# Optimization experiments

Measured on AMD Instinct MI355X. Metric: run time of the kernel, lower is better.

Reference implementation:

```python
import jax, jax.numpy as jnp
import numpy as np

N_ENT = 15000  # entity id range; also used for relation ids in this synthetic setup

def _triple_key(h, r, t):
    # Unique int64 key per (h, r, t) triple; max ~15000^3 < 2^63.
    return (h * N_ENT + r) * N_ENT + t

def setup_inputs() -> dict:
    key = jax.random.key(0)
    k1, k2, k3, k4 = jax.random.split(key, 4)
    Q, N = 100000, 10000000
    heads = jax.random.randint(k1, (Q,), 0, N_ENT, dtype=jnp.int64)
    rels = jax.random.randint(k2, (Q,), 0, N_ENT, dtype=jnp.int64)
    tails = jax.random.randint(k3, (Q,), 0, N_ENT, dtype=jnp.int64)
    data = jax.random.randint(k4, (3, N), 0, N_ENT, dtype=jnp.int64)
    return {"heads": heads, "rels": rels, "tails": tails, "data": data}

def reference(heads, rels, tails, data) -> jnp.ndarray:
    # Faithful to PerfeCT.forward: response[i] = 1 iff (heads[i], rels[i], tails[i])
    # appears as a row of data.T; output = 10 * (response - 0.5).
    data_keys = jnp.sort(_triple_key(data[0], data[1], data[2]))  # [N]
    q_keys = _triple_key(heads, rels, tails)                       # [Q]
    idx = jnp.searchsorted(data_keys, q_keys)
    idx = jnp.clip(idx, 0, data_keys.shape[0] - 1)
    member = (data_keys[idx] == q_keys).astype(jnp.float32)        # [Q]
    return 10.0 * (member - 0.5)
```

## Files before the change

kernel.cpp:

```cpp
#include <hip/hip_runtime.h>
#include <stdint.h>


typedef int iv4 __attribute__((ext_vector_type(4)));

#define EMPTY  0xFFFFFFFFu
#define BWORDS 32768
#define QSLOTS 6
#define TPB    1024

static __device__ __forceinline__ uint32_t mix32(uint32_t x) {
    x ^= x >> 16; x *= 0x85ebca6bu;
    x ^= x >> 13; x *= 0xc2b2ae35u;
    x ^= x >> 16;
    return x;
}
static __device__ __forceinline__ uint32_t hash2(uint32_t x) {
    return mix32(x ^ 0x9E3779B9u);
}
static __device__ __forceinline__ uint32_t key32(int h, int r, int t) {
    return ((uint32_t)h * 15000u + (uint32_t)r) * 15000u + (uint32_t)t;
}
static __device__ __forceinline__ void bloom_wm(uint32_t key, uint32_t* w, uint32_t* m) {
    uint32_t z = mix32(key);
    *w = z & (BWORDS - 1u);
    *m = (1u << ((z >> 15) & 31u)) | (1u << ((z >> 20) & 31u));
}

__global__ void k_zero(uint32_t* __restrict__ p, int zeroWords, int totalWords) {
    int stride = gridDim.x * blockDim.x;
    for (int i = blockIdx.x * blockDim.x + threadIdx.x; i < totalWords; i += stride)
        p[i] = (i < zeroWords) ? 0u : EMPTY;
}

__global__ void k_insert(const int* __restrict__ qh, const int* __restrict__ qr,
                         const int* __restrict__ qt,
                         uint32_t* __restrict__ bloom, uint32_t* __restrict__ keys,
                         uint32_t tmask, int Q) {
    int i = blockIdx.x * blockDim.x + threadIdx.x;
    if (i >= Q) return;
    uint32_t key = key32(qh[i], qr[i], qt[i]);
    if (key == EMPTY) return;
    uint32_t w, m; bloom_wm(key, &w, &m);
    atomicOr(&bloom[w], m);
    uint32_t slot = hash2(key) & tmask;
    while (true) {
        uint32_t prev = atomicCAS(&keys[slot], EMPTY, key);
        if (prev == EMPTY || prev == key) return;
        slot = (slot + 1) & tmask;
    }
}

static __device__ __forceinline__ void probe_mark(uint32_t key,
                                                  const uint32_t* __restrict__ keys,
                                                  uint32_t* __restrict__ flagbits,
                                                  uint32_t tmask) {
    uint32_t slot = hash2(key) & tmask;
    while (true) {
        uint32_t v = keys[slot];
        if (v == key) { atomicOr(&flagbits[slot >> 5], 1u << (slot & 31)); return; }
        if (v == EMPTY) return;
        slot = (slot + 1) & tmask;
    }
}

__global__ __launch_bounds__(TPB) void k_scan(
        const int* __restrict__ dh, const int* __restrict__ dr,
        const int* __restrict__ dt,
        const uint32_t* __restrict__ bloom,
        const uint32_t* __restrict__ keys,
        uint32_t* __restrict__ flagbits, uint32_t* __restrict__ sent,
        uint32_t tmask, int nhex, int N) {
    __shared__ uint32_t lb[BWORDS];
    __shared__ uint32_t qb[TPB * QSLOTS];
    {
        const iv4* gb = (const iv4*)bloom;
        iv4* lb4 = (iv4*)lb;
        for (int i = threadIdx.x; i < BWORDS / 4; i += TPB) lb4[i] = gb[i];
    }
    __syncthreads();

    const iv4* H = (const iv4*)dh;
    const iv4* R = (const iv4*)dr;
    const iv4* T = (const iv4*)dt;
    int cnt = 0;
    int stride = gridDim.x * blockDim.x;

#define TESTQ(kk, vv, mm)                                                          \
    if ((kk) == EMPTY) *sent = 1u;                                                 \
    else if (((vv) & (mm)) == (mm)) {                                              \
        if (cnt < QSLOTS) { qb[cnt * TPB + threadIdx.x] = (kk); cnt++; }           \
        else probe_mark((kk), keys, flagbits, tmask);                              \
    }
#define GRP4(h4, r4, t4)                                                           \
    {                                                                              \
        uint32_t k0 = key32((h4).x, (r4).x, (t4).x), k1 = key32((h4).y, (r4).y, (t4).y); \
        uint32_t k2 = key32((h4).z, (r4).z, (t4).z), k3 = key32((h4).w, (r4).w, (t4).w); \
        uint32_t w0,m0,w1,m1,w2,m2,w3,m3;                                          \
        bloom_wm(k0,&w0,&m0); bloom_wm(k1,&w1,&m1);                                \
        bloom_wm(k2,&w2,&m2); bloom_wm(k3,&w3,&m3);                                \
        uint32_t v0 = lb[w0], v1 = lb[w1], v2 = lb[w2], v3 = lb[w3];               \
        TESTQ(k0, v0, m0) TESTQ(k1, v1, m1) TESTQ(k2, v2, m2) TESTQ(k3, v3, m3)    \
    }

    for (int j = blockIdx.x * blockDim.x + threadIdx.x; j < nhex; j += stride) {
        iv4 hA = H[j], hB = H[j + nhex], hC = H[j + 2 * nhex], hD = H[j + 3 * nhex];
        iv4 rA = R[j], rB = R[j + nhex], rC = R[j + 2 * nhex], rD = R[j + 3 * nhex];
        iv4 tA = T[j], tB = T[j + nhex], tC = T[j + 2 * nhex], tD = T[j + 3 * nhex];
        GRP4(hA, rA, tA) GRP4(hB, rB, tB) GRP4(hC, rC, tC) GRP4(hD, rD, tD)
    }
#undef GRP4
#undef TESTQ

    int rem = N - 16 * nhex;
    if (blockIdx.x == 0 && (int)threadIdx.x < rem) {
        int j = 16 * nhex + threadIdx.x;
        uint32_t k = key32(dh[j], dr[j], dt[j]);
        if (k == EMPTY) *sent = 1u;
        else probe_mark(k, keys, flagbits, tmask);
    }

    int m = cnt < QSLOTS ? cnt : QSLOTS;
    for (int c = 0; c < m; ++c)
        probe_mark(qb[c * TPB + threadIdx.x], keys, flagbits, tmask);
}

__global__ void k_out(const int* __restrict__ qh, const int* __restrict__ qr,
                      const int* __restrict__ qt,
                      const uint32_t* __restrict__ keys,
                      const uint32_t* __restrict__ flagbits,
                      const uint32_t* __restrict__ sent,
                      float* __restrict__ out, uint32_t tmask, int Q) {
    int i = blockIdx.x * blockDim.x + threadIdx.x;
    if (i >= Q) return;
    uint32_t key = key32(qh[i], qr[i], qt[i]);
    float v = -5.0f;
    if (key == EMPTY) {
        v = (*sent) ? 5.0f : -5.0f;
    } else {
        uint32_t slot = hash2(key) & tmask;
        while (true) {
            uint32_t kv = keys[slot];
            if (kv == key) { v = ((flagbits[slot >> 5] >> (slot & 31)) & 1u) ? 5.0f : -5.0f; break; }
            if (kv == EMPTY) break;
            slot = (slot + 1) & tmask;
        }
    }
    out[i] = v;
}

extern "C" void kernel_launch(void* const* d_in, const int* in_sizes, int n_in,
                              void* d_out, int out_size, void* d_ws, size_t ws_size,
                              hipStream_t stream) {
    const int* qh = (const int*)d_in[0];
    const int* qr = (const int*)d_in[1];
    const int* qt = (const int*)d_in[2];
    const int* data = (const int*)d_in[3];
    int Q = in_sizes[0];
    int N = in_sizes[3] / 3;
    const int* dh = data;
    const int* dr = data + (size_t)N;
    const int* dt = data + 2 * (size_t)N;
    float* out = (float*)d_out;

    int tb = 18;
    size_t bloomB = (size_t)BWORDS * 4;
    size_t need = bloomB + ((size_t)1 << (tb - 3)) + 256 + ((size_t)4 << tb);
    if (need > ws_size) tb = 17;
    size_t flagB = (size_t)1 << (tb - 3);
    uint32_t tmask = ((uint32_t)1 << tb) - 1u;

    uint32_t* bloom    = (uint32_t*)d_ws;
    uint32_t* flagbits = (uint32_t*)((char*)d_ws + bloomB);
    uint32_t* hdr      = (uint32_t*)((char*)d_ws + bloomB + flagB);
    uint32_t* keys     = (uint32_t*)((char*)d_ws + bloomB + flagB + 256);

    int zeroWords  = (int)((bloomB + flagB + 256) / 4);
    int totalWords = zeroWords + (1 << tb);
    k_zero<<<1024, 256, 0, stream>>>((uint32_t*)d_ws, zeroWords, totalWords);

    int qblocks = (Q + 255) / 256;
    k_insert<<<qblocks, 256, 0, stream>>>(qh, qr, qt, bloom, keys, tmask, Q);

    int nhex = N / 16;
    k_scan<<<256, TPB, 0, stream>>>(dh, dr, dt, bloom, keys, flagbits,
                                    hdr, tmask, nhex, N);

    k_out<<<qblocks, 256, 0, stream>>>(qh, qr, qt, keys, flagbits, hdr, out, tmask, Q);
}
```

Before: 222.0 us.

## Shrink bloom filter, keep probe queue in registers, raise scan occupancy

Halves the shared-memory bloom filter and replaces the shared-memory deferred-probe queue with six registers, so more scan blocks can reside per CU. The per-thread unroll drops from 16 to 8 elements, the grid doubles, and streaming loads use nontemporal hints. The goal is better latency hiding in the scan. The smaller bloom raises the false-positive rate, so more rows fall through to global hash-table probes.

```diff
diff --git a/kernel.cpp b/kernel.cpp
--- a/kernel.cpp
+++ b/kernel.cpp
@@ -5,8 +5,7 @@
 typedef int iv4 __attribute__((ext_vector_type(4)));
 
 #define EMPTY  0xFFFFFFFFu
-#define BWORDS 32768
-#define QSLOTS 6
+#define BWORDS 16384
 #define TPB    1024
 
 static __device__ __forceinline__ uint32_t mix32(uint32_t x) {
@@ -24,7 +23,7 @@
 static __device__ __forceinline__ void bloom_wm(uint32_t key, uint32_t* w, uint32_t* m) {
     uint32_t z = mix32(key);
     *w = z & (BWORDS - 1u);
-    *m = (1u << ((z >> 15) & 31u)) | (1u << ((z >> 20) & 31u));
+    *m = (1u << ((z >> 14) & 31u)) | (1u << ((z >> 19) & 31u));
 }
 
 __global__ void k_zero(uint32_t* __restrict__ p, int zeroWords, int totalWords) {
@@ -64,15 +63,14 @@
     }
 }
 
-__global__ __launch_bounds__(TPB) void k_scan(
+__global__ __launch_bounds__(TPB, 8) void k_scan(
         const int* __restrict__ dh, const int* __restrict__ dr,
         const int* __restrict__ dt,
         const uint32_t* __restrict__ bloom,
         const uint32_t* __restrict__ keys,
         uint32_t* __restrict__ flagbits, uint32_t* __restrict__ sent,
-        uint32_t tmask, int nhex, int N) {
+        uint32_t tmask, int n8, int N) {
     __shared__ uint32_t lb[BWORDS];
-    __shared__ uint32_t qb[TPB * QSLOTS];
     {
         const iv4* gb = (const iv4*)bloom;
         iv4* lb4 = (iv4*)lb;
@@ -84,12 +82,13 @@
     const iv4* R = (const iv4*)dr;
     const iv4* T = (const iv4*)dt;
     int cnt = 0;
+    uint32_t q0 = 0, q1 = 0, q2 = 0, q3 = 0, q4 = 0, q5 = 0;
     int stride = gridDim.x * blockDim.x;
 
 #define TESTQ(kk, vv, mm)                                                          \
     if ((kk) == EMPTY) *sent = 1u;                                                 \
     else if (((vv) & (mm)) == (mm)) {                                              \
-        if (cnt < QSLOTS) { qb[cnt * TPB + threadIdx.x] = (kk); cnt++; }           \
+        if (cnt < 6) { q5 = q4; q4 = q3; q3 = q2; q2 = q1; q1 = q0; q0 = (kk); cnt++; } \
         else probe_mark((kk), keys, flagbits, tmask);                              \
     }
 #define GRP4(h4, r4, t4)                                                           \
@@ -103,26 +102,32 @@
         TESTQ(k0, v0, m0) TESTQ(k1, v1, m1) TESTQ(k2, v2, m2) TESTQ(k3, v3, m3)    \
     }
 
-    for (int j = blockIdx.x * blockDim.x + threadIdx.x; j < nhex; j += stride) {
-        iv4 hA = H[j], hB = H[j + nhex], hC = H[j + 2 * nhex], hD = H[j + 3 * nhex];
-        iv4 rA = R[j], rB = R[j + nhex], rC = R[j + 2 * nhex], rD = R[j + 3 * nhex];
-        iv4 tA = T[j], tB = T[j + nhex], tC = T[j + 2 * nhex], tD = T[j + 3 * nhex];
-        GRP4(hA, rA, tA) GRP4(hB, rB, tB) GRP4(hC, rC, tC) GRP4(hD, rD, tD)
+    for (int j = blockIdx.x * blockDim.x + threadIdx.x; j < n8; j += stride) {
+        iv4 hA = __builtin_nontemporal_load(&H[j]);
+        iv4 hB = __builtin_nontemporal_load(&H[j + n8]);
+        iv4 rA = __builtin_nontemporal_load(&R[j]);
+        iv4 rB = __builtin_nontemporal_load(&R[j + n8]);
+        iv4 tA = __builtin_nontemporal_load(&T[j]);
+        iv4 tB = __builtin_nontemporal_load(&T[j + n8]);
+        GRP4(hA, rA, tA) GRP4(hB, rB, tB)
     }
 #undef GRP4
 #undef TESTQ
 
-    int rem = N - 16 * nhex;
+    int rem = N - 8 * n8;
     if (blockIdx.x == 0 && (int)threadIdx.x < rem) {
-        int j = 16 * nhex + threadIdx.x;
+        int j = 8 * n8 + threadIdx.x;
         uint32_t k = key32(dh[j], dr[j], dt[j]);
         if (k == EMPTY) *sent = 1u;
         else probe_mark(k, keys, flagbits, tmask);
     }
 
-    int m = cnt < QSLOTS ? cnt : QSLOTS;
-    for (int c = 0; c < m; ++c)
-        probe_mark(qb[c * TPB + threadIdx.x], keys, flagbits, tmask);
+    if (cnt > 0) probe_mark(q0, keys, flagbits, tmask);
+    if (cnt > 1) probe_mark(q1, keys, flagbits, tmask);
+    if (cnt > 2) probe_mark(q2, keys, flagbits, tmask);
+    if (cnt > 3) probe_mark(q3, keys, flagbits, tmask);
+    if (cnt > 4) probe_mark(q4, keys, flagbits, tmask);
+    if (cnt > 5) probe_mark(q5, keys, flagbits, tmask);
 }
 
 __global__ void k_out(const int* __restrict__ qh, const int* __restrict__ qr,
@@ -182,9 +187,9 @@
     int qblocks = (Q + 255) / 256;
     k_insert<<<qblocks, 256, 0, stream>>>(qh, qr, qt, bloom, keys, tmask, Q);
 
-    int nhex = N / 16;
-    k_scan<<<256, TPB, 0, stream>>>(dh, dr, dt, bloom, keys, flagbits,
-                                    hdr, tmask, nhex, N);
+    int n8 = N / 8;
+    k_scan<<<512, TPB, 0, stream>>>(dh, dr, dt, bloom, keys, flagbits,
+                                    hdr, tmask, n8, N);
 
     k_out<<<qblocks, 256, 0, stream>>>(qh, qr, qt, keys, flagbits, hdr, out, tmask, Q);
 }
```

Result: faster. 209.3 us (-5.7%).
